# Kernel optimization log

Measured on AMD Instinct MI355X. Metric: run time of the kernel, lower is better.

## Reference

```python
import jax, jax.numpy as jnp
import numpy as np

N = 4096  # out_features (rows of W)
M = 4096  # in_features (cols of W)
S = 2048  # number of Givens pairs per side (= N//2)
TOKENS = 2048
EPS = 1e-8


def setup_inputs() -> dict:
    key = jax.random.key(0)
    ks = jax.random.split(key, 6)
    x = jax.random.normal(ks[0], (TOKENS, M), dtype=jnp.float32)
    W = jax.random.normal(ks[1], (N, M), dtype=jnp.float32) * (1.0 / np.sqrt(M))
    bias = jax.random.normal(ks[2], (N,), dtype=jnp.float32) * 0.02
    theta_L = 0.02 * jax.random.normal(ks[3], (S,), dtype=jnp.float32)
    theta_R = 0.02 * jax.random.normal(ks[4], (S,), dtype=jnp.float32)
    ecd_log_mag = jnp.zeros((N,), dtype=jnp.float32)
    # disjoint index pairs: (0,1),(2,3),... as produced by a permutation reshape
    pairs_L = jnp.arange(N, dtype=jnp.int64).reshape(S, 2)
    pairs_R = jnp.arange(M, dtype=jnp.int64).reshape(S, 2)
    return {"x": x, "W": W, "bias": bias, "theta_L": theta_L,
            "theta_R": theta_R, "ecd_log_mag": ecd_log_mag,
            "pairs_L": pairs_L, "pairs_R": pairs_R}


def _apply_left_rotations(W, theta, pairs):
    # Plane (Givens) rotations on disjoint row pairs of W: [S] angles, [S,2] indices
    c = jnp.cos(theta)[:, None]
    s = jnp.sin(theta)[:, None]
    i, j = pairs[:, 0], pairs[:, 1]
    ri, rj = W[i], W[j]                       # [S, M] gathers
    return W.at[i].set(c * ri - s * rj).at[j].set(s * ri + c * rj)


def _apply_right_rotations(W, theta, pairs):
    # Plane rotations on disjoint column pairs of W
    c = jnp.cos(theta)
    s = jnp.sin(theta)
    p, q = pairs[:, 0], pairs[:, 1]
    cp, cq = W[:, p], W[:, q]                 # [N, S] gathers
    return W.at[:, p].set(c * cp - s * cq).at[:, q].set(s * cp + c * cq)


def reference(x, W, bias, theta_L, theta_R, ecd_log_mag, pairs_L, pairs_R):
    # base row norms are buffers computed under no_grad from the frozen base weight
    base_row_norms = jax.lax.stop_gradient(jnp.linalg.norm(W, axis=1))  # [N]
    Wp = _apply_left_rotations(W, theta_L, pairs_L)
    Wp = _apply_right_rotations(Wp, theta_R, pairs_R)
    # magnitude rescale: row-normalize rotated weight, scale by learned magnitude
    row_norm = jnp.linalg.norm(Wp, axis=1, keepdims=True)               # [N,1]
    mag = base_row_norms * jnp.exp(ecd_log_mag)                         # [N]
    W_eff = Wp * (mag[:, None] / (row_norm + EPS))                      # [N,M]
    return x @ W_eff.T + bias                                           # [T,N]
```

## Files before the change

### kernel.cpp

```cpp
#include <hip/hip_runtime.h>
#include <hip/hip_bf16.h>


#define GK 4096
#define GN 4096
#define GT 2048
#define NPAIR 2048

typedef __bf16 bf16x8 __attribute__((ext_vector_type(8)));
typedef float  f32x4  __attribute__((ext_vector_type(4)));

static __device__ __forceinline__ unsigned short f2bf(float f) {
    union { float f; unsigned int u; } v; v.f = f;
    unsigned int r = v.u + 0x7fffu + ((v.u >> 16) & 1u);
    return (unsigned short)(r >> 16);
}
static __device__ __forceinline__ unsigned int pack2bf(float a, float b) {
    return (unsigned int)f2bf(a) | ((unsigned int)f2bf(b) << 16);
}

static __device__ __forceinline__ void sincos_poly(float t, float* s, float* c) {
    const float t2 = t * t;
    *s = t * (1.f + t2 * (-0.16666667f + t2 * 8.3333338e-3f));
    *c = 1.f + t2 * (-0.5f + t2 * (4.1666668e-2f + t2 * -1.3888889e-3f));
}

__global__ __launch_bounds__(256) void prelude(
    const float* __restrict__ W, const float* __restrict__ thL,
    const float* __restrict__ thR, const float* __restrict__ ecd,
    const float* __restrict__ x,
    unsigned short* __restrict__ Weff, unsigned short* __restrict__ Xbf)
{
    const int tid = threadIdx.x;

    if (blockIdx.x >= 2048) {
        const int cb = blockIdx.x - 2048;
        const size_t base = (size_t)cb * 512;
        const float4* X4 = (const float4*)x;
        uint4* O4 = (uint4*)Xbf;
#pragma unroll
        for (int k = 0; k < 2; k++) {
            const size_t m = base + tid + k * 256;
            const float4 a = X4[2 * m];
            const float4 b = X4[2 * m + 1];
            uint4 o;
            o.x = pack2bf(a.x, a.y);
            o.y = pack2bf(a.z, a.w);
            o.z = pack2bf(b.x, b.y);
            o.w = pack2bf(b.z, b.w);
            O4[m] = o;
        }
        return;
    }

    const int s  = blockIdx.x;
    const int i0 = 2 * s, i1 = 2 * s + 1;

    float cL, sL;
    sincos_poly(thL[s], &sL, &cL);

    float4 b0[4], b1[4];
    float s00 = 0.f, s11 = 0.f, s01 = 0.f;

    const float4* r0 = (const float4*)(W + (size_t)i0 * GK);
    const float4* r1 = (const float4*)(W + (size_t)i1 * GK);
    const float2* T2 = (const float2*)thR;

#pragma unroll
    for (int k = 0; k < 4; k++) {
        const int c4 = tid + k * 256;
        const float4 w0 = r0[c4];
        const float4 w1 = r1[c4];
        const float2 tt = T2[c4];
        float4 cs;
        sincos_poly(tt.x, &cs.y, &cs.x);
        sincos_poly(tt.y, &cs.w, &cs.z);
        s00 += w0.x * w0.x + w0.y * w0.y + w0.z * w0.z + w0.w * w0.w;
        s11 += w1.x * w1.x + w1.y * w1.y + w1.z * w1.z + w1.w * w1.w;
        s01 += w0.x * w1.x + w0.y * w1.y + w0.z * w1.z + w0.w * w1.w;
        const float a0x = cL * w0.x - sL * w1.x;
        const float a0y = cL * w0.y - sL * w1.y;
        const float a0z = cL * w0.z - sL * w1.z;
        const float a0w = cL * w0.w - sL * w1.w;
        const float a1x = sL * w0.x + cL * w1.x;
        const float a1y = sL * w0.y + cL * w1.y;
        const float a1z = sL * w0.z + cL * w1.z;
        const float a1w = sL * w0.w + cL * w1.w;
        b0[k].x = cs.x * a0x - cs.y * a0y;
        b0[k].y = cs.y * a0x + cs.x * a0y;
        b0[k].z = cs.z * a0z - cs.w * a0w;
        b0[k].w = cs.w * a0z + cs.z * a0w;
        b1[k].x = cs.x * a1x - cs.y * a1y;
        b1[k].y = cs.y * a1x + cs.x * a1y;
        b1[k].z = cs.z * a1z - cs.w * a1w;
        b1[k].w = cs.w * a1z + cs.z * a1w;
    }

#pragma unroll
    for (int off = 32; off; off >>= 1) {
        s00 += __shfl_down(s00, off);
        s11 += __shfl_down(s11, off);
        s01 += __shfl_down(s01, off);
    }
    __shared__ float red[3][4];
    __shared__ float scales[2];
    const int wave = tid >> 6, lane = tid & 63;
    if (lane == 0) { red[0][wave] = s00; red[1][wave] = s11; red[2][wave] = s01; }
    __syncthreads();
    if (tid == 0) {
        const float t0 = red[0][0] + red[0][1] + red[0][2] + red[0][3];
        const float t1 = red[1][0] + red[1][1] + red[1][2] + red[1][3];
        const float td = red[2][0] + red[2][1] + red[2][2] + red[2][3];
        const float n0 = cL * cL * t0 + sL * sL * t1 - 2.f * cL * sL * td;
        const float n1 = sL * sL * t0 + cL * cL * t1 + 2.f * cL * sL * td;
        scales[0] = sqrtf(t0) * expf(ecd[i0]) / (sqrtf(n0) + 1e-8f);
        scales[1] = sqrtf(t1) * expf(ecd[i1]) / (sqrtf(n1) + 1e-8f);
    }
    __syncthreads();
    const float sc0 = scales[0], sc1 = scales[1];

    uint2* o0 = (uint2*)(Weff + (size_t)i0 * GK);
    uint2* o1 = (uint2*)(Weff + (size_t)i1 * GK);
#pragma unroll
    for (int k = 0; k < 4; k++) {
        const int c4 = tid + k * 256;
        uint2 p0, p1;
        p0.x = pack2bf(b0[k].x * sc0, b0[k].y * sc0);
        p0.y = pack2bf(b0[k].z * sc0, b0[k].w * sc0);
        p1.x = pack2bf(b1[k].x * sc1, b1[k].y * sc1);
        p1.y = pack2bf(b1[k].z * sc1, b1[k].w * sc1);
        o0[c4] = p0;
        o1[c4] = p1;
    }
}

static __device__ __forceinline__ void glds16(const unsigned short* g, unsigned short* l) {
    __builtin_amdgcn_global_load_lds(
        (const __attribute__((address_space(1))) unsigned int*)g,
        (__attribute__((address_space(3))) unsigned int*)l, 16, 0, 0);
}

__global__ __launch_bounds__(512, 4) void gemm_bt(
    const unsigned short* __restrict__ A,
    const unsigned short* __restrict__ B,
    const float* __restrict__ bias,
    float* __restrict__ C)
{
    constexpr int BM = 128, BN = 128, BK = 64;
    constexpr int NT = GK / BK;
    __shared__ unsigned short smem[2][2][BM * BK];

    const int tid  = threadIdx.x;
    const int lane = tid & 63;
    const int wave = tid >> 6;
    const int quad = lane >> 4;
    const int l16  = lane & 15;
    const int wm   = wave >> 2;
    const int wn   = wave & 3;
    const int bm   = blockIdx.y * BM;
    const int bn   = blockIdx.x * BN;

    const float bv0 = bias[bn + wn * 32 + 0 * 16 + l16];
    const float bv1 = bias[bn + wn * 32 + 1 * 16 + l16];

    const int lrow = lane >> 3;
    const int jlog = (lane & 7) ^ lrow;
    const unsigned short* gA[2];
    const unsigned short* gB[2];
    int loff[2];
#pragma unroll
    for (int j = 0; j < 2; j++) {
        const int c = 2 * wave + j;
        gA[j] = A + (size_t)(bm + c * 8 + lrow) * GK + jlog * 8;
        gB[j] = B + (size_t)(bn + c * 8 + lrow) * GK + jlog * 8;
        loff[j] = c * 512 + lane * 8;
    }

#define STAGE(buf, k0) do {                                               \
    _Pragma("unroll")                                                     \
    for (int j = 0; j < 2; j++) {                                         \
        glds16(gA[j] + (k0), &smem[buf][0][loff[j]]);                     \
        glds16(gB[j] + (k0), &smem[buf][1][loff[j]]);                     \
    } } while (0)

    f32x4 acc[4][2] = {};

#define COMPUTE(b) do {                                                   \
    const unsigned short* As_ = &smem[b][0][0];                           \
    const unsigned short* Bs_ = &smem[b][1][0];                           \
    bf16x8 aF[2][4], bF[2][2];                                            \
    _Pragma("unroll")                                                     \
    for (int kk = 0; kk < 2; kk++) {                                      \
        const int ps = ((quad + 4 * kk) ^ (l16 & 7)) * 8;                 \
        _Pragma("unroll")                                                 \
        for (int i = 0; i < 4; i++)                                       \
            aF[kk][i] = *(const bf16x8*)(As_ + (wm * 64 + i * 16 + l16) * BK + ps); \
        _Pragma("unroll")                                                 \
        for (int j = 0; j < 2; j++)                                       \
            bF[kk][j] = *(const bf16x8*)(Bs_ + (wn * 32 + j * 16 + l16) * BK + ps); \
    }                                                                     \
    _Pragma("unroll")                                                     \
    for (int i = 0; i < 4; i++) {                                         \
        _Pragma("unroll")                                                 \
        for (int j = 0; j < 2; j++) {                                     \
            acc[i][j] = __builtin_amdgcn_mfma_f32_16x16x32_bf16(          \
                aF[0][i], bF[0][j], acc[i][j], 0, 0, 0);                  \
            acc[i][j] = __builtin_amdgcn_mfma_f32_16x16x32_bf16(          \
                aF[1][i], bF[1][j], acc[i][j], 0, 0, 0);                  \
        } }                                                               \
    } while (0)

    STAGE(0, 0);
    int cur = 0;
    for (int t = 0; t < NT - 1; ++t) {
        STAGE(cur ^ 1, (t + 1) * BK);
        __builtin_amdgcn_sched_barrier(0);
        asm volatile("s_waitcnt vmcnt(4)" ::: "memory");
        __builtin_amdgcn_s_barrier();
        __builtin_amdgcn_sched_barrier(0);
        COMPUTE(cur);
        __builtin_amdgcn_sched_barrier(0);
        __builtin_amdgcn_s_barrier();
        cur ^= 1;
    }
    asm volatile("s_waitcnt vmcnt(0)" ::: "memory");
    __builtin_amdgcn_s_barrier();
    __builtin_amdgcn_sched_barrier(0);
    COMPUTE(cur);

#undef STAGE
#undef COMPUTE

#pragma unroll
    for (int i = 0; i < 4; i++) {
        const int m = bm + wm * 64 + i * 16 + quad * 4;
        const int n0 = bn + wn * 32 + l16;
#pragma unroll
        for (int r = 0; r < 4; r++) {
            C[(size_t)(m + r) * GN + n0]      = acc[i][0][r] + bv0;
            C[(size_t)(m + r) * GN + n0 + 16] = acc[i][1][r] + bv1;
        }
    }
}

extern "C" void kernel_launch(void* const* d_in, const int* in_sizes, int n_in,
                              void* d_out, int out_size, void* d_ws, size_t ws_size,
                              hipStream_t stream) {
    const float* x    = (const float*)d_in[0];
    const float* W    = (const float*)d_in[1];
    const float* bias = (const float*)d_in[2];
    const float* thL  = (const float*)d_in[3];
    const float* thR  = (const float*)d_in[4];
    const float* ecd  = (const float*)d_in[5];

    unsigned short* Weff = (unsigned short*)d_ws;
    unsigned short* Xbf  = (unsigned short*)((char*)d_ws + (size_t)GN * GK * 2);

    float* out = (float*)d_out;

    prelude<<<dim3(4096), dim3(256), 0, stream>>>(W, thL, thR, ecd, x, Weff, Xbf);
    gemm_bt<<<dim3(GN / 128, GT / 128), dim3(512), 0, stream>>>(Xbf, Weff, bias, out);
}
```

Baseline: 206.9 us.

## Pre-pack activations into MFMA fragment order and load A directly to registers

```diff
diff --git a/kernel.cpp b/kernel.cpp
--- a/kernel.cpp
+++ b/kernel.cpp
@@ -35,20 +35,26 @@
 
     if (blockIdx.x >= 2048) {
         const int cb = blockIdx.x - 2048;
-        const size_t base = (size_t)cb * 512;
         const float4* X4 = (const float4*)x;
         uint4* O4 = (uint4*)Xbf;
 #pragma unroll
         for (int k = 0; k < 2; k++) {
-            const size_t m = base + tid + k * 256;
-            const float4 a = X4[2 * m];
-            const float4 b = X4[2 * m + 1];
+            const int c  = cb * 512 + tid + k * 256;
+            const int r  = c & 15;
+            const int q  = (c >> 4) & 3;
+            const int kk = (c >> 6) & 1;
+            const int t  = (c >> 7) & 63;
+            const int I  = c >> 13;
+            const int m  = I * 16 + r;
+            const int k4 = t * 16 + kk * 8 + q * 2;
+            const float4 a = X4[(size_t)m * (GK / 4) + k4];
+            const float4 b = X4[(size_t)m * (GK / 4) + k4 + 1];
             uint4 o;
             o.x = pack2bf(a.x, a.y);
             o.y = pack2bf(a.z, a.w);
             o.z = pack2bf(b.x, b.y);
             o.w = pack2bf(b.z, b.w);
-            O4[m] = o;
+            O4[c] = o;
         }
         return;
     }
@@ -148,7 +154,7 @@
 {
     constexpr int BM = 128, BN = 128, BK = 64;
     constexpr int NT = GK / BK;
-    __shared__ unsigned short smem[2][2][BM * BK];
+    __shared__ unsigned short sB[2][BN * BK];
 
     const int tid  = threadIdx.x;
     const int lane = tid & 63;
@@ -165,36 +171,44 @@
 
     const int lrow = lane >> 3;
     const int jlog = (lane & 7) ^ lrow;
-    const unsigned short* gA[2];
     const unsigned short* gB[2];
     int loff[2];
 #pragma unroll
     for (int j = 0; j < 2; j++) {
         const int c = 2 * wave + j;
-        gA[j] = A + (size_t)(bm + c * 8 + lrow) * GK + jlog * 8;
         gB[j] = B + (size_t)(bn + c * 8 + lrow) * GK + jlog * 8;
         loff[j] = c * 512 + lane * 8;
     }
 
-#define STAGE(buf, k0) do {                                               \
-    _Pragma("unroll")                                                     \
-    for (int j = 0; j < 2; j++) {                                         \
-        glds16(gA[j] + (k0), &smem[buf][0][loff[j]]);                     \
-        glds16(gB[j] + (k0), &smem[buf][1][loff[j]]);                     \
+    const unsigned short* Afrag[4];
+#pragma unroll
+    for (int i = 0; i < 4; i++)
+        Afrag[i] = A + (size_t)(blockIdx.y * 8 + wm * 4 + i) * 65536 + lane * 8;
+
+#define STAGE_B(buf, k0) do {                                             \
+    _Pragma("unroll")                                                     \
+    for (int j = 0; j < 2; j++)                                           \
+        glds16(gB[j] + (k0), &sB[buf][loff[j]]);                          \
+    } while (0)
+
+#define A_LOADS(t) do {                                                   \
+    _Pragma("unroll")                                                     \
+    for (int i = 0; i < 4; i++) {                                         \
+        asm volatile("global_load_dwordx4 %0, %1, off"                    \
+            : "=&v"(aF[0][i]) : "v"(Afrag[i] + (t) * 1024));              \
+        asm volatile("global_load_dwordx4 %0, %1, off"                    \
+            : "=&v"(aF[1][i]) : "v"(Afrag[i] + (t) * 1024 + 512));        \
     } } while (0)
 
     f32x4 acc[4][2] = {};
+    bf16x8 aF[2][4];
 
 #define COMPUTE(b) do {                                                   \
-    const unsigned short* As_ = &smem[b][0][0];                           \
-    const unsigned short* Bs_ = &smem[b][1][0];                           \
-    bf16x8 aF[2][4], bF[2][2];                                            \
+    const unsigned short* Bs_ = &sB[b][0];                                \
+    bf16x8 bF[2][2];                                                      \
     _Pragma("unroll")                                                     \
     for (int kk = 0; kk < 2; kk++) {                                      \
         const int ps = ((quad + 4 * kk) ^ (l16 & 7)) * 8;                 \
-        _Pragma("unroll")                                                 \
-        for (int i = 0; i < 4; i++)                                       \
-            aF[kk][i] = *(const bf16x8*)(As_ + (wm * 64 + i * 16 + l16) * BK + ps); \
         _Pragma("unroll")                                                 \
         for (int j = 0; j < 2; j++)                                       \
             bF[kk][j] = *(const bf16x8*)(Bs_ + (wn * 32 + j * 16 + l16) * BK + ps); \
@@ -210,25 +224,32 @@
         } }                                                               \
     } while (0)
 
-    STAGE(0, 0);
+    STAGE_B(0, 0);
+    A_LOADS(0);
+
     int cur = 0;
-    for (int t = 0; t < NT - 1; ++t) {
-        STAGE(cur ^ 1, (t + 1) * BK);
+    for (int t = 0; t < NT; ++t) {
+        if (t < NT - 1) STAGE_B(cur ^ 1, (t + 1) * BK);
         __builtin_amdgcn_sched_barrier(0);
-        asm volatile("s_waitcnt vmcnt(4)" ::: "memory");
+        if (t < NT - 1) {
+            asm volatile("s_waitcnt vmcnt(2)" ::: "memory");
+        } else {
+            asm volatile("s_waitcnt vmcnt(0)" ::: "memory");
+        }
         __builtin_amdgcn_s_barrier();
         __builtin_amdgcn_sched_barrier(0);
         COMPUTE(cur);
         __builtin_amdgcn_sched_barrier(0);
-        __builtin_amdgcn_s_barrier();
+        if (t < NT - 1) {
+            A_LOADS(t + 1);
+            __builtin_amdgcn_sched_barrier(0);
+            __builtin_amdgcn_s_barrier();
+        }
         cur ^= 1;
     }
-    asm volatile("s_waitcnt vmcnt(0)" ::: "memory");
-    __builtin_amdgcn_s_barrier();
-    __builtin_amdgcn_sched_barrier(0);
-    COMPUTE(cur);
-
-#undef STAGE
+
+#undef STAGE_B
+#undef A_LOADS
 #undef COMPUTE
 
 #pragma unroll
```

Measured after the change: 231.7 us. +12.0%, slower.
